# Kernel optimization log

Measured on AMD Instinct MI355X. Metric: run time of the kernel, lower is better.

Reference implementation:

```python
import jax, jax.numpy as jnp
import numpy as np
import math

B, S, H = 2, 2048, 1024
NH, HD = 16, 64
EPS = 1e-12


def setup_inputs() -> dict:
    key = jax.random.key(0)
    ks = jax.random.split(key, 6)
    scale = 1.0 / math.sqrt(H)
    return {
        "hidden_states": jax.random.normal(ks[0], (B, S, H), jnp.float32),
        "Wq": jax.random.normal(ks[1], (H, H), jnp.float32) * scale,
        "bq": jnp.zeros((H,), jnp.float32),
        "Wk": jax.random.normal(ks[2], (H, H), jnp.float32) * scale,
        "bk": jnp.zeros((H,), jnp.float32),
        "Wv": jax.random.normal(ks[3], (H, H), jnp.float32) * scale,
        "bv": jnp.zeros((H,), jnp.float32),
        "Wo": jax.random.normal(ks[4], (H, H), jnp.float32) * scale,
        "bo": jnp.zeros((H,), jnp.float32),
        "gamma": jnp.ones((H,), jnp.float32),
        "beta": jnp.zeros((H,), jnp.float32),
    }


def _heads(x):
    # [B, S, H] -> [B, NH, S, HD]
    return x.reshape(B, S, NH, HD).transpose(0, 2, 1, 3)


def reference(hidden_states, Wq, bq, Wk, bk, Wv, bv, Wo, bo, gamma, beta):
    q = _heads(hidden_states @ Wq + bq)
    k = _heads(hidden_states @ Wk + bk)
    v = _heads(hidden_states @ Wv + bv)
    # scores: [B, NH, S, S]
    scores = jnp.einsum("bhqd,bhkd->bhqk", q, k) / math.sqrt(HD)
    probs = jax.nn.softmax(scores, axis=-1)
    ctx = jnp.einsum("bhqk,bhkd->bhqd", probs, v)
    ctx = ctx.transpose(0, 2, 1, 3).reshape(B, S, H)
    attn_out = ctx @ Wo + bo
    x = attn_out + hidden_states
    mu = jnp.mean(x, axis=-1, keepdims=True)
    var = jnp.var(x, axis=-1, keepdims=True)
    return (x - mu) / jnp.sqrt(var + EPS) * gamma + beta
```

## Files before the change

kernel.cpp:

```cpp
#include <hip/hip_runtime.h>
#include <hip/hip_bf16.h>

#define B_ 2
#define S_ 2048
#define H_ 1024
#define NH_ 16
#define HD_ 64
#define M_ (B_*S_)

typedef __attribute__((ext_vector_type(8))) short bf16x8;
typedef __attribute__((ext_vector_type(4))) short bf16x4;
typedef __attribute__((ext_vector_type(4))) float f32x4;
typedef __attribute__((ext_vector_type(4))) int   i32x4;

__device__ inline float waveReduceSum(float v) {
#pragma unroll
  for (int off = 32; off >= 1; off >>= 1) v += __shfl_xor(v, off);
  return v;
}

__device__ inline short f2bf(float f) {
  union { float f; unsigned u; } v; v.f = f;
  unsigned r = v.u + 0x7fffu + ((v.u >> 16) & 1u);
  return (short)(r >> 16);
}

__device__ inline unsigned cvt_pk_bf16(float lo, float hi) {
  unsigned w;
  asm("v_cvt_pk_bf16_f32 %0, %1, %2" : "=v"(w) : "v"(lo), "v"(hi));
  return w;
}

__device__ inline void async_load16(const void* g, void* l) {
  __builtin_amdgcn_global_load_lds(
      (const __attribute__((address_space(1))) void*)g,
      (__attribute__((address_space(3))) void*)l, 16, 0, 0);
}

__global__ __launch_bounds__(256)
void cvt_bf16(const float* __restrict__ in, short* __restrict__ out) {
  const size_t i = (size_t)blockIdx.x * 256 + threadIdx.x;
  float4 v = ((const float4*)in)[i];
  bf16x4 o;
  o[0] = f2bf(v.x); o[1] = f2bf(v.y); o[2] = f2bf(v.z); o[3] = f2bf(v.w);
  ((bf16x4*)out)[i] = o;
}

__global__ __launch_bounds__(256)
void transpose_w4(const float* __restrict__ W0, const float* __restrict__ W1,
                  const float* __restrict__ W2, const float* __restrict__ W3,
                  short* __restrict__ Tqkv, short* __restrict__ To) {
  const float* W; short* T;
  switch (blockIdx.z) {
    case 0: W = W0; T = Tqkv; break;
    case 1: W = W1; T = Tqkv + (size_t)1024 * 1024; break;
    case 2: W = W2; T = Tqkv + (size_t)2048 * 1024; break;
    default: W = W3; T = To; break;
  }
  __shared__ float tile[32][36];
  const int tid = threadIdx.x;
  const int tx = tid & 7, ty = tid >> 3;
  const int k0 = blockIdx.y << 5, n0 = blockIdx.x << 5;
  float4 v = *(const float4*)&W[(size_t)(k0 + ty) * H_ + n0 + (tx << 2)];
  tile[ty][(tx << 2) + 0] = v.x;
  tile[ty][(tx << 2) + 1] = v.y;
  tile[ty][(tx << 2) + 2] = v.z;
  tile[ty][(tx << 2) + 3] = v.w;
  __syncthreads();
  bf16x4 o;
  o[0] = f2bf(tile[(tx << 2) + 0][ty]);
  o[1] = f2bf(tile[(tx << 2) + 1][ty]);
  o[2] = f2bf(tile[(tx << 2) + 2][ty]);
  o[3] = f2bf(tile[(tx << 2) + 3][ty]);
  *(bf16x4*)&T[(size_t)(n0 + ty) * H_ + k0 + (tx << 2)] = o;
}

__global__ __launch_bounds__(256)
void gemm_qkv(const short* __restrict__ A, const short* __restrict__ Bt,
              const float* __restrict__ bq, const float* __restrict__ bk,
              const float* __restrict__ bv, short* __restrict__ Qo,
              short* __restrict__ Ko, short* __restrict__ Vto) {
  __shared__ short A_lds[2][128][32];
  __shared__ short B_lds[2][128][32];
  const int tid = threadIdx.x;
  const int lane = tid & 63, wv = tid >> 6;
  const int l16 = lane & 15, lg = lane >> 4;
  const int wr = wv >> 1, wc = wv & 1;
  const int swzb = (blockIdx.x & 7) * 96 + (blockIdx.x >> 3);
  const int bx = swzb % 24, by = swzb / 24;
  const int m0 = by << 7, n0 = bx << 7;
  const int K = H_;

  const int srow = lane >> 2, soff = (lane & 3) << 3;

  f32x4 acc[4][4] = {};

#pragma unroll
  for (int i = 0; i < 2; ++i) {
    const int c = 2 * wv + i;
    async_load16(A + (size_t)(m0 + 16 * c + srow) * K + soff, &A_lds[0][16 * c][0]);
    async_load16(Bt + (size_t)(n0 + 16 * c + srow) * K + soff, &B_lds[0][16 * c][0]);
  }

  int cur = 0;
  for (int t = 0; t < K / 32; ++t) {
    __syncthreads();
    if (t + 1 < K / 32) {
      const int k0 = (t + 1) << 5;
#pragma unroll
      for (int i = 0; i < 2; ++i) {
        const int c = 2 * wv + i;
        async_load16(A + (size_t)(m0 + 16 * c + srow) * K + k0 + soff,
                     &A_lds[cur ^ 1][16 * c][0]);
        async_load16(Bt + (size_t)(n0 + 16 * c + srow) * K + k0 + soff,
                     &B_lds[cur ^ 1][16 * c][0]);
      }
    }
    bf16x8 af[4], bfr[4];
#pragma unroll
    for (int i = 0; i < 4; ++i)
      af[i] = *(const bf16x8*)&A_lds[cur][64 * wr + 16 * i + l16][8 * lg];
#pragma unroll
    for (int j = 0; j < 4; ++j)
      bfr[j] = *(const bf16x8*)&B_lds[cur][64 * wc + 16 * j + l16][8 * lg];
#pragma unroll
    for (int i = 0; i < 4; ++i)
#pragma unroll
      for (int j = 0; j < 4; ++j)
        acc[i][j] = __builtin_amdgcn_mfma_f32_16x16x32_bf16(af[i], bfr[j], acc[i][j], 0, 0, 0);
    cur ^= 1;
  }

  const int mt = n0 >> 10;
  const float* bias = (mt == 0) ? bq : (mt == 1 ? bk : bv);
  const float qs = (mt == 0) ? 0.125f : 1.0f;

  if (mt < 2) {
    short* Out = (mt == 0) ? Qo : Ko;
#pragma unroll
    for (int i = 0; i < 4; ++i) {
#pragma unroll
      for (int j = 0; j < 4; ++j) {
        const int nl = (n0 & 1023) + 64 * wc + 16 * j + l16;
        const float bvl = bias[nl];
        const int h = nl >> 6, d = nl & 63;
#pragma unroll
        for (int r = 0; r < 4; ++r) {
          const int m = m0 + 64 * wr + 16 * i + 4 * lg + r;
          const int b = m >> 11, s = m & (S_ - 1);
          Out[(((size_t)(b * NH_ + h) * S_ + s) << 6) + d] =
              f2bf((acc[i][j][r] + bvl) * qs);
        }
      }
    }
  } else {
#pragma unroll
    for (int i = 0; i < 4; ++i) {
      const int mb = m0 + 64 * wr + 16 * i + 4 * lg;
      const int b = mb >> 11, s = mb & (S_ - 1);
#pragma unroll
      for (int j = 0; j < 4; ++j) {
        const int nl = (n0 & 1023) + 64 * wc + 16 * j + l16;
        const float bvl = bias[nl];
        const int h = nl >> 6, d = nl & 63;
        bf16x4 pk;
#pragma unroll
        for (int r = 0; r < 4; ++r) pk[r] = f2bf(acc[i][j][r] + bvl);
        *(bf16x4*)&Vto[(((size_t)(b * NH_ + h) * HD_ + d) << 11) + s] = pk;
      }
    }
  }
}

__global__ __launch_bounds__(256)
void gemm_o(const short* __restrict__ A, const short* __restrict__ Bt,
            const float* __restrict__ bias, float* __restrict__ C) {
  __shared__ short A_lds[2][128][32];
  __shared__ short B_lds[2][128][32];
  const int tid = threadIdx.x;
  const int lane = tid & 63, wv = tid >> 6;
  const int l16 = lane & 15, lg = lane >> 4;
  const int wr = wv >> 1, wc = wv & 1;
  const int swzb = (blockIdx.x & 7) * 32 + (blockIdx.x >> 3);
  const int bx = swzb & 7, by = swzb >> 3;
  const int m0 = by << 7, n0 = bx << 7;
  const int K = H_;

  const int srow = lane >> 2, soff = (lane & 3) << 3;

  f32x4 acc[4][4] = {};

#pragma unroll
  for (int i = 0; i < 2; ++i) {
    const int c = 2 * wv + i;
    async_load16(A + (size_t)(m0 + 16 * c + srow) * K + soff, &A_lds[0][16 * c][0]);
    async_load16(Bt + (size_t)(n0 + 16 * c + srow) * K + soff, &B_lds[0][16 * c][0]);
  }

  int cur = 0;
  for (int t = 0; t < K / 32; ++t) {
    __syncthreads();
    if (t + 1 < K / 32) {
      const int k0 = (t + 1) << 5;
#pragma unroll
      for (int i = 0; i < 2; ++i) {
        const int c = 2 * wv + i;
        async_load16(A + (size_t)(m0 + 16 * c + srow) * K + k0 + soff,
                     &A_lds[cur ^ 1][16 * c][0]);
        async_load16(Bt + (size_t)(n0 + 16 * c + srow) * K + k0 + soff,
                     &B_lds[cur ^ 1][16 * c][0]);
      }
    }
    bf16x8 af[4], bfr[4];
#pragma unroll
    for (int i = 0; i < 4; ++i)
      af[i] = *(const bf16x8*)&A_lds[cur][64 * wr + 16 * i + l16][8 * lg];
#pragma unroll
    for (int j = 0; j < 4; ++j)
      bfr[j] = *(const bf16x8*)&B_lds[cur][64 * wc + 16 * j + l16][8 * lg];
#pragma unroll
    for (int i = 0; i < 4; ++i)
#pragma unroll
      for (int j = 0; j < 4; ++j)
        acc[i][j] = __builtin_amdgcn_mfma_f32_16x16x32_bf16(af[i], bfr[j], acc[i][j], 0, 0, 0);
    cur ^= 1;
  }

#pragma unroll
  for (int i = 0; i < 4; ++i)
#pragma unroll
    for (int j = 0; j < 4; ++j) {
      const int n = n0 + 64 * wc + 16 * j + l16;
      const float bvl = bias[n];
#pragma unroll
      for (int r = 0; r < 4; ++r) {
        const int m = m0 + 64 * wr + 16 * i + 4 * lg + r;
        C[(size_t)m * H_ + n] = acc[i][j][r] + bvl;
      }
    }
}

#define KVB 64
#define LDK 72

__global__ __launch_bounds__(256)
void attn_mfma(const short* __restrict__ Qg, const short* __restrict__ Kg,
               const short* __restrict__ Vtg, short* __restrict__ ctxb) {
  __shared__ short K_lds[2][KVB][LDK];
  __shared__ short V_t[2][KVB][LDK];

  const int tid  = threadIdx.x;
  const int lane = tid & 63;
  const int wv   = tid >> 6;
  const int l16  = lane & 15, lg = lane >> 4;

  const int swz = (blockIdx.x & 7) * 128 + (blockIdx.x >> 3);
  const int bh = swz >> 5, qb = swz & 31;

  const short* Qh = Qg + ((size_t)bh * S_ << 6);
  const short* Kh = Kg + ((size_t)bh * S_ << 6);
  const short* Vh = Vtg + ((size_t)bh << 6) * S_;

  const int q0 = qb * 64 + wv * 16;

  bf16x8 qf[2];
  qf[0] = *(const bf16x8*)&Qh[((size_t)(q0 + l16) << 6) + 8 * lg];
  qf[1] = *(const bf16x8*)&Qh[((size_t)(q0 + l16) << 6) + 8 * lg + 32];

  const int kr = tid >> 2, d0 = (tid & 3) << 4;
  const int l16part = ((l16 >> 2) << 3) + (l16 & 3);

  f32x4 o[4] = {};
  float m_run = -1e30f, l_run = 0.f;

  {
    *(bf16x8*)&K_lds[0][kr][d0]     = *(const bf16x8*)&Kh[((size_t)kr << 6) + d0];
    *(bf16x8*)&K_lds[0][kr][d0 + 8] = *(const bf16x8*)&Kh[((size_t)kr << 6) + d0 + 8];
    *(bf16x8*)&V_t[0][kr][d0]       = *(const bf16x8*)&Vh[(size_t)kr * S_ + d0];
    *(bf16x8*)&V_t[0][kr][d0 + 8]   = *(const bf16x8*)&Vh[(size_t)kr * S_ + d0 + 8];
  }

  int cur = 0;
  for (int t = 0; t < S_ / KVB; ++t) {
    bf16x8 nk0, nk1, nv0, nv1;
    const bool pre = (t + 1 < S_ / KVB);
    if (pre) {
      const size_t kb = (size_t)((t + 1) * KVB + kr) << 6;
      nk0 = *(const bf16x8*)&Kh[kb + d0];
      nk1 = *(const bf16x8*)&Kh[kb + d0 + 8];
      const size_t vb = (size_t)kr * S_ + (t + 1) * KVB;
      nv0 = *(const bf16x8*)&Vh[vb + d0];
      nv1 = *(const bf16x8*)&Vh[vb + d0 + 8];
    }
    __syncthreads();

    f32x4 s[4] = {};
#pragma unroll
    for (int ks = 0; ks < 2; ++ks)
#pragma unroll
      for (int tt = 0; tt < 4; ++tt) {
        const int krow = ((tt >> 1) << 5) + ((tt & 1) << 2) + l16part;
        bf16x8 kf = *(const bf16x8*)&K_lds[cur][krow][8 * lg + 32 * ks];
        s[tt] = __builtin_amdgcn_mfma_f32_16x16x32_bf16(kf, qf[ks], s[tt], 0, 0, 0);
      }

    float pmax = fmaxf(fmaxf(fmaxf(s[0][0], s[0][1]), fmaxf(s[0][2], s[0][3])),
                       fmaxf(fmaxf(s[1][0], s[1][1]), fmaxf(s[1][2], s[1][3])));
    pmax = fmaxf(pmax,
                 fmaxf(fmaxf(fmaxf(s[2][0], s[2][1]), fmaxf(s[2][2], s[2][3])),
                       fmaxf(fmaxf(s[3][0], s[3][1]), fmaxf(s[3][2], s[3][3]))));
    pmax = fmaxf(pmax, __shfl_xor(pmax, 16));
    pmax = fmaxf(pmax, __shfl_xor(pmax, 32));

    const float mn = fmaxf(m_run, pmax);
    const float scl = __expf(m_run - mn);
    m_run = mn;

    float p[4][4];
    float rs = 0.f;
#pragma unroll
    for (int tt = 0; tt < 4; ++tt)
#pragma unroll
      for (int r = 0; r < 4; ++r) {
        p[tt][r] = __expf(s[tt][r] - mn);
        rs += p[tt][r];
      }
    rs += __shfl_xor(rs, 16);
    rs += __shfl_xor(rs, 32);
    l_run = l_run * scl + rs;

    unsigned w[4][2];
#pragma unroll
    for (int tt = 0; tt < 4; ++tt) {
      w[tt][0] = cvt_pk_bf16(p[tt][0], p[tt][1]);
      w[tt][1] = cvt_pk_bf16(p[tt][2], p[tt][3]);
    }

    float sclr[4];
#pragma unroll
    for (int r = 0; r < 4; ++r) sclr[r] = __shfl(scl, 20 * lg + r);
#pragma unroll
    for (int tt = 0; tt < 4; ++tt)
#pragma unroll
      for (int r = 0; r < 4; ++r) o[tt][r] *= sclr[r];

#pragma unroll
    for (int ks = 0; ks < 2; ++ks) {
      i32x4 aw;
      aw[0] = (int)w[2 * ks][0];
      aw[1] = (int)w[2 * ks][1];
      aw[2] = (int)w[2 * ks + 1][0];
      aw[3] = (int)w[2 * ks + 1][1];
      const bf16x8 pf = __builtin_bit_cast(bf16x8, aw);
#pragma unroll
      for (int tt = 0; tt < 4; ++tt) {
        bf16x8 vf = *(const bf16x8*)&V_t[cur][16 * tt + l16][8 * lg + 32 * ks];
        o[tt] = __builtin_amdgcn_mfma_f32_16x16x32_bf16(pf, vf, o[tt], 0, 0, 0);
      }
    }

    if (pre) {
      *(bf16x8*)&K_lds[cur ^ 1][kr][d0]     = nk0;
      *(bf16x8*)&K_lds[cur ^ 1][kr][d0 + 8] = nk1;
      *(bf16x8*)&V_t[cur ^ 1][kr][d0]       = nv0;
      *(bf16x8*)&V_t[cur ^ 1][kr][d0 + 8]   = nv1;
    }
    cur ^= 1;
  }

  float invr[4];
#pragma unroll
  for (int r = 0; r < 4; ++r) invr[r] = 1.f / __shfl(l_run, 20 * lg + r);
  const int b = bh >> 4, h = bh & 15;
#pragma unroll
  for (int r = 0; r < 4; ++r) {
    const int q = q0 + 4 * lg + r;
#pragma unroll
    for (int tt = 0; tt < 4; ++tt)
      ctxb[(((size_t)(b * S_ + q) * NH_ + h) << 6) + 16 * tt + l16] =
          f2bf(o[tt][r] * invr[r]);
  }
}

__global__ __launch_bounds__(256)
void resid_ln(const float* __restrict__ attn_out, const float* __restrict__ hs,
              const float* __restrict__ gamma, const float* __restrict__ beta,
              float* __restrict__ out) {
  __shared__ float reds[4], reds2[4];
  const int row = blockIdx.x;
  const int tid = threadIdx.x;
  const float4* a4 = (const float4*)(attn_out + ((size_t)row << 10));
  const float4* h4 = (const float4*)(hs + ((size_t)row << 10));
  float4 a = a4[tid], h = h4[tid];
  float e0 = a.x + h.x, e1 = a.y + h.y, e2 = a.z + h.z, e3 = a.w + h.w;
  float s  = e0 + e1 + e2 + e3;
  float sq = e0 * e0 + e1 * e1 + e2 * e2 + e3 * e3;
  s = waveReduceSum(s);
  sq = waveReduceSum(sq);
  const int lane = tid & 63, wave = tid >> 6;
  if (lane == 0) { reds[wave] = s; reds2[wave] = sq; }
  __syncthreads();
  const float S1 = reds[0] + reds[1] + reds[2] + reds[3];
  const float S2 = reds2[0] + reds2[1] + reds2[2] + reds2[3];
  const float mu = S1 * (1.f / H_);
  const float var = S2 * (1.f / H_) - mu * mu;
  const float rstd = rsqrtf(var + 1e-12f);
  const float4 g = ((const float4*)gamma)[tid];
  const float4 bb = ((const float4*)beta)[tid];
  float4 o;
  o.x = (e0 - mu) * rstd * g.x + bb.x;
  o.y = (e1 - mu) * rstd * g.y + bb.y;
  o.z = (e2 - mu) * rstd * g.z + bb.z;
  o.w = (e3 - mu) * rstd * g.w + bb.w;
  ((float4*)(out + ((size_t)row << 10)))[tid] = o;
}

extern "C" void kernel_launch(void* const* d_in, const int* in_sizes, int n_in,
                              void* d_out, int out_size, void* d_ws, size_t ws_size,
                              hipStream_t stream) {
  const float* X     = (const float*)d_in[0];
  const float* Wq    = (const float*)d_in[1];
  const float* bq    = (const float*)d_in[2];
  const float* Wk    = (const float*)d_in[3];
  const float* bk    = (const float*)d_in[4];
  const float* Wv    = (const float*)d_in[5];
  const float* bv    = (const float*)d_in[6];
  const float* Wo    = (const float*)d_in[7];
  const float* bo    = (const float*)d_in[8];
  const float* gamma = (const float*)d_in[9];
  const float* beta  = (const float*)d_in[10];
  float* out = (float*)d_out;

  char* ws = (char*)d_ws;
  short* Xbf  = (short*)ws;
  short* Wqkv = (short*)(ws + ( 8u << 20));
  short* Wto  = (short*)(ws + (14u << 20));
  short* Qbf  = (short*)(ws + (16u << 20));
  short* Kbf  = (short*)(ws + (24u << 20));
  short* Vt   = (short*)(ws + (32u << 20));
  short* ctxb = Xbf;
  float* attn = (float*)(ws + (16u << 20));

  dim3 blk(256);
  hipLaunchKernelGGL(cvt_bf16, dim3((M_ * H_) / 1024), blk, 0, stream, X, Xbf);
  hipLaunchKernelGGL(transpose_w4, dim3(32, 32, 4), blk, 0, stream,
                     Wq, Wk, Wv, Wo, Wqkv, Wto);
  hipLaunchKernelGGL(gemm_qkv, dim3(768), blk, 0, stream,
                     Xbf, Wqkv, bq, bk, bv, Qbf, Kbf, Vt);
  hipLaunchKernelGGL(attn_mfma, dim3(1024), blk, 0, stream, Qbf, Kbf, Vt, ctxb);
  hipLaunchKernelGGL(gemm_o, dim3(256), blk, 0, stream, ctxb, Wto, bo, attn);
  hipLaunchKernelGGL(resid_ln, dim3(M_), blk, 0, stream, attn, X, gamma, beta, out);
}
```

Baseline: 255.6 us.

## Stream K/V into swizzled LDS via async loads and use lazy exp2 softmax rescaling

The attention kernel now stages K and V tiles with global_load_lds async copies into unpadded LDS tiles using an XOR chunk swizzle, replacing register-staged prefetch and padded rows. The softmax folds log2(e) into the Q scale and uses exp2, and it skips the running-max rescale of the output accumulators unless some lane's max grows by more than 8. The shuffle source lane for the per-row scale and sum also changes. This aims to cut LDS bank conflicts, register pressure and per-tile rescale work, at the cost of more complex indexing and a bounded growth of unnormalised probabilities.

```diff
diff --git a/kernel.cpp b/kernel.cpp
--- a/kernel.cpp
+++ b/kernel.cpp
@@ -36,6 +36,8 @@
       (const __attribute__((address_space(1))) void*)g,
       (__attribute__((address_space(3))) void*)l, 16, 0, 0);
 }
+
+__device__ inline int swz8(int r) { return (r & 3) | (((r >> 3) & 1) << 2); }
 
 __global__ __launch_bounds__(256)
 void cvt_bf16(const float* __restrict__ in, short* __restrict__ out) {
@@ -133,7 +135,7 @@
 
   const int mt = n0 >> 10;
   const float* bias = (mt == 0) ? bq : (mt == 1 ? bk : bv);
-  const float qs = (mt == 0) ? 0.125f : 1.0f;
+  const float qs = (mt == 0) ? 0.125f * 1.4426950408889634f : 1.0f;
 
   if (mt < 2) {
     short* Out = (mt == 0) ? Qo : Ko;
@@ -241,13 +243,12 @@
 }
 
 #define KVB 64
-#define LDK 72
 
 __global__ __launch_bounds__(256)
 void attn_mfma(const short* __restrict__ Qg, const short* __restrict__ Kg,
                const short* __restrict__ Vtg, short* __restrict__ ctxb) {
-  __shared__ short K_lds[2][KVB][LDK];
-  __shared__ short V_t[2][KVB][LDK];
+  __shared__ short K_lds[2][KVB][64];
+  __shared__ short V_t[2][KVB][64];
 
   const int tid  = threadIdx.x;
   const int lane = tid & 63;
@@ -267,32 +268,33 @@
   qf[0] = *(const bf16x8*)&Qh[((size_t)(q0 + l16) << 6) + 8 * lg];
   qf[1] = *(const bf16x8*)&Qh[((size_t)(q0 + l16) << 6) + 8 * lg + 32];
 
-  const int kr = tid >> 2, d0 = (tid & 3) << 4;
   const int l16part = ((l16 >> 2) << 3) + (l16 & 3);
+
+  const int srow8 = lane >> 3;
+  const int schk  = lane & 7;
 
   f32x4 o[4] = {};
   float m_run = -1e30f, l_run = 0.f;
 
-  {
-    *(bf16x8*)&K_lds[0][kr][d0]     = *(const bf16x8*)&Kh[((size_t)kr << 6) + d0];
-    *(bf16x8*)&K_lds[0][kr][d0 + 8] = *(const bf16x8*)&Kh[((size_t)kr << 6) + d0 + 8];
-    *(bf16x8*)&V_t[0][kr][d0]       = *(const bf16x8*)&Vh[(size_t)kr * S_ + d0];
-    *(bf16x8*)&V_t[0][kr][d0 + 8]   = *(const bf16x8*)&Vh[(size_t)kr * S_ + d0 + 8];
-  }
+#define STAGE(buf, kv0)                                                        \
+  {                                                                            \
+    _Pragma("unroll")                                                          \
+    for (int i_ = 0; i_ < 2; ++i_) {                                           \
+      const int row_ = 16 * wv + 8 * i_ + srow8;                               \
+      const int ch_ = schk ^ swz8(row_);                                       \
+      async_load16(Kh + (((size_t)((kv0) + row_)) << 6) + (ch_ << 3),          \
+                   &K_lds[buf][16 * wv + 8 * i_][0]);                          \
+      async_load16(Vh + (size_t)row_ * S_ + (kv0) + (ch_ << 3),                \
+                   &V_t[buf][16 * wv + 8 * i_][0]);                            \
+    }                                                                          \
+  }
+
+  STAGE(0, 0)
 
   int cur = 0;
   for (int t = 0; t < S_ / KVB; ++t) {
-    bf16x8 nk0, nk1, nv0, nv1;
-    const bool pre = (t + 1 < S_ / KVB);
-    if (pre) {
-      const size_t kb = (size_t)((t + 1) * KVB + kr) << 6;
-      nk0 = *(const bf16x8*)&Kh[kb + d0];
-      nk1 = *(const bf16x8*)&Kh[kb + d0 + 8];
-      const size_t vb = (size_t)kr * S_ + (t + 1) * KVB;
-      nv0 = *(const bf16x8*)&Vh[vb + d0];
-      nv1 = *(const bf16x8*)&Vh[vb + d0 + 8];
-    }
     __syncthreads();
+    if (t + 1 < S_ / KVB) STAGE(cur ^ 1, (t + 1) * KVB)
 
     f32x4 s[4] = {};
 #pragma unroll
@@ -300,7 +302,8 @@
 #pragma unroll
       for (int tt = 0; tt < 4; ++tt) {
         const int krow = ((tt >> 1) << 5) + ((tt & 1) << 2) + l16part;
-        bf16x8 kf = *(const bf16x8*)&K_lds[cur][krow][8 * lg + 32 * ks];
+        const int kch = (lg + 4 * ks) ^ swz8(krow);
+        bf16x8 kf = *(const bf16x8*)&K_lds[cur][krow][kch << 3];
         s[tt] = __builtin_amdgcn_mfma_f32_16x16x32_bf16(kf, qf[ks], s[tt], 0, 0, 0);
       }
 
@@ -312,22 +315,41 @@
     pmax = fmaxf(pmax, __shfl_xor(pmax, 16));
     pmax = fmaxf(pmax, __shfl_xor(pmax, 32));
 
-    const float mn = fmaxf(m_run, pmax);
-    const float scl = __expf(m_run - mn);
-    m_run = mn;
-
     float p[4][4];
     float rs = 0.f;
-#pragma unroll
-    for (int tt = 0; tt < 4; ++tt)
-#pragma unroll
-      for (int r = 0; r < 4; ++r) {
-        p[tt][r] = __expf(s[tt][r] - mn);
-        rs += p[tt][r];
-      }
-    rs += __shfl_xor(rs, 16);
-    rs += __shfl_xor(rs, 32);
-    l_run = l_run * scl + rs;
+    if (__any(pmax - m_run > 8.0f)) {
+      const float mn = fmaxf(m_run, pmax);
+      const float scl = __builtin_amdgcn_exp2f(m_run - mn);
+      m_run = mn;
+#pragma unroll
+      for (int tt = 0; tt < 4; ++tt)
+#pragma unroll
+        for (int r = 0; r < 4; ++r) {
+          p[tt][r] = __builtin_amdgcn_exp2f(s[tt][r] - mn);
+          rs += p[tt][r];
+        }
+      rs += __shfl_xor(rs, 16);
+      rs += __shfl_xor(rs, 32);
+      l_run = l_run * scl + rs;
+      float sclr[4];
+#pragma unroll
+      for (int r = 0; r < 4; ++r) sclr[r] = __shfl(scl, 4 * lg + r);
+#pragma unroll
+      for (int tt = 0; tt < 4; ++tt)
+#pragma unroll
+        for (int r = 0; r < 4; ++r) o[tt][r] *= sclr[r];
+    } else {
+#pragma unroll
+      for (int tt = 0; tt < 4; ++tt)
+#pragma unroll
+        for (int r = 0; r < 4; ++r) {
+          p[tt][r] = __builtin_amdgcn_exp2f(s[tt][r] - m_run);
+          rs += p[tt][r];
+        }
+      rs += __shfl_xor(rs, 16);
+      rs += __shfl_xor(rs, 32);
+      l_run += rs;
+    }
 
     unsigned w[4][2];
 #pragma unroll
@@ -335,14 +357,6 @@
       w[tt][0] = cvt_pk_bf16(p[tt][0], p[tt][1]);
       w[tt][1] = cvt_pk_bf16(p[tt][2], p[tt][3]);
     }
-
-    float sclr[4];
-#pragma unroll
-    for (int r = 0; r < 4; ++r) sclr[r] = __shfl(scl, 20 * lg + r);
-#pragma unroll
-    for (int tt = 0; tt < 4; ++tt)
-#pragma unroll
-      for (int r = 0; r < 4; ++r) o[tt][r] *= sclr[r];
 
 #pragma unroll
     for (int ks = 0; ks < 2; ++ks) {
@@ -354,23 +368,19 @@
       const bf16x8 pf = __builtin_bit_cast(bf16x8, aw);
 #pragma unroll
       for (int tt = 0; tt < 4; ++tt) {
-        bf16x8 vf = *(const bf16x8*)&V_t[cur][16 * tt + l16][8 * lg + 32 * ks];
+        const int vrow = 16 * tt + l16;
+        const int vch = (lg + 4 * ks) ^ swz8(vrow);
+        bf16x8 vf = *(const bf16x8*)&V_t[cur][vrow][vch << 3];
         o[tt] = __builtin_amdgcn_mfma_f32_16x16x32_bf16(pf, vf, o[tt], 0, 0, 0);
       }
     }
-
-    if (pre) {
-      *(bf16x8*)&K_lds[cur ^ 1][kr][d0]     = nk0;
-      *(bf16x8*)&K_lds[cur ^ 1][kr][d0 + 8] = nk1;
-      *(bf16x8*)&V_t[cur ^ 1][kr][d0]       = nv0;
-      *(bf16x8*)&V_t[cur ^ 1][kr][d0 + 8]   = nv1;
-    }
     cur ^= 1;
   }
+#undef STAGE
 
   float invr[4];
 #pragma unroll
-  for (int r = 0; r < 4; ++r) invr[r] = 1.f / __shfl(l_run, 20 * lg + r);
+  for (int r = 0; r < 4; ++r) invr[r] = 1.f / __shfl(l_run, 4 * lg + r);
   const int b = bh >> 4, h = bh & 15;
 #pragma unroll
   for (int r = 0; r < 4; ++r) {
```

New measurement: 269.5 us. 5.4% more time.
